# Kernel tuning notes

Measured on AMD Instinct MI355X. Metric: run time of the kernel, lower is better.

The kernel has to match this reference:

```python
import jax, jax.numpy as jnp
import numpy as np
import math

D_MODEL = 7168
NUM_HEADS = 128
Q_LORA = 1536
KV_LORA = 512
DN = 128   # qk_nope_head_dim
DR = 64    # qk_rope_head_dim
DV = 128   # v_head_dim
DQ = DN + DR  # q_head_dim = 192
ROPE_BASE = 10000.0


def _apply_rotary(t, cos, sin):
    """Faithful port of apply_rotary_pos_emb (interleaved even/odd split).
    t: [B,H,S,DR]; cos,sin: [S,DR]."""
    cos = cos[None, None]  # [1,1,S,DR]
    sin = sin[None, None]
    x1 = t[..., ::2]
    x2 = t[..., 1::2]
    c = cos[..., ::2]
    s = sin[..., ::2]
    rot = jnp.stack([x1 * c - x2 * s, x1 * s + x2 * c], axis=-1)
    return rot.reshape(t.shape)


def setup_inputs() -> dict:
    key = jax.random.key(0)
    ks = jax.random.split(key, 7)
    B, S = 1, 1024
    sc = 0.02  # small init to keep softmax well-conditioned
    hidden_states = jax.random.normal(ks[0], (B, S, D_MODEL), dtype=jnp.float32)
    Wqa = jax.random.normal(ks[1], (Q_LORA, D_MODEL), dtype=jnp.float32) * sc
    Wkva = jax.random.normal(ks[2], (KV_LORA, D_MODEL), dtype=jnp.float32) * sc
    Wqb = jax.random.normal(ks[3], (NUM_HEADS * DQ, Q_LORA), dtype=jnp.float32) * sc
    Wkb = jax.random.normal(ks[4], (NUM_HEADS * DQ, KV_LORA), dtype=jnp.float32) * sc
    Wvb = jax.random.normal(ks[5], (NUM_HEADS * DV, KV_LORA), dtype=jnp.float32) * sc
    Wo = jax.random.normal(ks[6], (D_MODEL, NUM_HEADS * DV), dtype=jnp.float32) * sc
    return {"hidden_states": hidden_states, "Wqa": Wqa, "Wkva": Wkva,
            "Wqb": Wqb, "Wkb": Wkb, "Wvb": Wvb, "Wo": Wo}


def reference(hidden_states, Wqa, Wkva, Wqb, Wkb, Wvb, Wo):
    B, S, _ = hidden_states.shape
    # low-rank latent projections
    q_lat = jnp.einsum('bsd,rd->bsr', hidden_states, Wqa)    # [B,S,Q_LORA]
    kv_lat = jnp.einsum('bsd,rd->bsr', hidden_states, Wkva)  # [B,S,KV_LORA]
    # per-head up-projections
    q = jnp.einsum('bsr,er->bse', q_lat, Wqb).reshape(B, S, NUM_HEADS, DQ).transpose(0, 2, 1, 3)
    k = jnp.einsum('bsr,er->bse', kv_lat, Wkb).reshape(B, S, NUM_HEADS, DQ).transpose(0, 2, 1, 3)
    v = jnp.einsum('bsr,er->bse', kv_lat, Wvb).reshape(B, S, NUM_HEADS, DV).transpose(0, 2, 1, 3)
    # RoPE tables (YaRoPE: emb = cat(freqs, freqs))
    pos = jnp.arange(S, dtype=jnp.float32)
    inv_freq = 1.0 / (ROPE_BASE ** (jnp.arange(0, DR, 2, dtype=jnp.float32) / DR))
    freqs = jnp.outer(pos, inv_freq)                  # [S, DR/2]
    emb = jnp.concatenate([freqs, freqs], axis=-1)    # [S, DR]
    cos, sin = jnp.cos(emb), jnp.sin(emb)
    # split nope / rope, rotate rope halves
    q_nope, q_rope = q[..., :DN], q[..., DN:]
    k_nope, k_rope = k[..., :DN], k[..., DN:]
    q_rope = _apply_rotary(q_rope, cos, sin)
    k_rope = _apply_rotary(k_rope, cos, sin)
    q = jnp.concatenate([q_nope, q_rope], axis=-1)
    k = jnp.concatenate([k_nope, k_rope], axis=-1)
    # attention (no mask: attention_mask=None path)
    scores = jnp.einsum('bhqd,bhkd->bhqk', q, k) / math.sqrt(DQ)
    attn = jax.nn.softmax(scores, axis=-1)
    out = jnp.einsum('bhqk,bhkd->bhqd', attn, v)      # [B,H,S,DV]
    out = out.transpose(0, 2, 1, 3).reshape(B, S, NUM_HEADS * DV)
    return jnp.einsum('bse,de->bsd', out, Wo)         # [B,S,D_MODEL]
```

## Files before the change

### kernel.cpp

```cpp
#include <hip/hip_runtime.h>

typedef short v8s __attribute__((ext_vector_type(8)));
typedef float v4f __attribute__((ext_vector_type(4)));

#define S_LEN 1024
#define NH    128
#define DM    7168
#define QL    1536
#define KVL   512
#define DQd   192
#define DVd   128
#define QDIM  (NH * DQd)
#define VDIM  (NH * DVd)

__device__ __forceinline__ float bf2f(unsigned short u) {
  union { unsigned int i; float f; } x; x.i = ((unsigned int)u) << 16; return x.f;
}
__device__ __forceinline__ unsigned short f2bf(float f) {
  union { float f; unsigned int i; } x; x.f = f;
  unsigned int r = x.i + 0x7fffu + ((x.i >> 16) & 1u);
  return (unsigned short)(r >> 16);
}
__device__ __forceinline__ v8s cvt8pair(v4f f0, v4f f1) {
  v8s r; unsigned short* u = (unsigned short*)&r;
#pragma unroll
  for (int i = 0; i < 4; i++) { u[i] = f2bf(f0[i]); u[4 + i] = f2bf(f1[i]); }
  return r;
}

__device__ __forceinline__ int swz_off(int row, int slot) {
  return row * 128 + ((slot ^ (row & 7)) << 4);
}

__global__ void cvt_bf16_kernel(const float* __restrict__ in,
                                unsigned short* __restrict__ out, int n8) {
  int i = blockIdx.x * blockDim.x + threadIdx.x;
  if (i >= n8) return;
  v4f f0 = *(const v4f*)(in + (size_t)i * 8);
  v4f f1 = *(const v4f*)(in + (size_t)i * 8 + 4);
  *(v8s*)(out + (size_t)i * 8) = cvt8pair(f0, f1);
}

template<bool CF32>
__global__ __launch_bounds__(256) void gemm_tile(
    const unsigned short* __restrict__ A, int lda,
    const float* __restrict__ W, int ldw,
    void* __restrict__ Cv, int ldc, int K)
{
  __shared__ __align__(16) unsigned short As[128 * 64];
  __shared__ __align__(16) unsigned short Bs[128 * 64];

  const int t    = threadIdx.x;
  const int lane = t & 63;
  const int wave = t >> 6;
  const int r15  = lane & 15;
  const int quad = lane >> 4;
  const int wm = wave >> 1, wn = wave & 1;
  const int mb = blockIdx.y * 128;
  const int nb = blockIdx.x * 128;

  const int srow  = t >> 3;
  const int sslot = t & 7;

  const unsigned short* aptr = A + (size_t)(mb + srow) * lda + sslot * 8;
  const float*          wptr = W + (size_t)(nb + srow) * ldw + sslot * 8;
  const size_t a32 = (size_t)32 * lda;
  const size_t w32 = (size_t)32 * ldw;

  v4f acc[4][4];
#pragma unroll
  for (int i = 0; i < 4; i++)
#pragma unroll
    for (int j = 0; j < 4; j++) acc[i][j] = (v4f){0.f, 0.f, 0.f, 0.f};

  v8s stA[4];
  v4f stB[8];
#pragma unroll
  for (int p = 0; p < 4; p++) stA[p] = *(const v8s*)(aptr + p * a32);
#pragma unroll
  for (int p = 0; p < 4; p++) {
    stB[2 * p]     = *(const v4f*)(wptr + p * w32);
    stB[2 * p + 1] = *(const v4f*)(wptr + p * w32 + 4);
  }

  for (int k0 = 0; k0 < K; k0 += 64) {
    __syncthreads();
#pragma unroll
    for (int p = 0; p < 4; p++)
      *(v8s*)((char*)As + swz_off(p * 32 + srow, sslot)) = stA[p];
#pragma unroll
    for (int p = 0; p < 4; p++)
      *(v8s*)((char*)Bs + swz_off(p * 32 + srow, sslot)) =
          cvt8pair(stB[2 * p], stB[2 * p + 1]);
    __syncthreads();

    if (k0 + 64 < K) {
#pragma unroll
      for (int p = 0; p < 4; p++)
        stA[p] = *(const v8s*)(aptr + p * a32 + k0 + 64);
#pragma unroll
      for (int p = 0; p < 4; p++) {
        stB[2 * p]     = *(const v4f*)(wptr + p * w32 + k0 + 64);
        stB[2 * p + 1] = *(const v4f*)(wptr + p * w32 + k0 + 64 + 4);
      }
    }

#pragma unroll
    for (int kk = 0; kk < 2; kk++) {
      const int cslot = kk * 4 + quad;
      v8s af[4], bf[4];
#pragma unroll
      for (int fm = 0; fm < 4; fm++)
        af[fm] = *(const v8s*)((char*)As + swz_off(wm * 64 + fm * 16 + r15, cslot));
#pragma unroll
      for (int fn = 0; fn < 4; fn++)
        bf[fn] = *(const v8s*)((char*)Bs + swz_off(wn * 64 + fn * 16 + r15, cslot));
#pragma unroll
      for (int fm = 0; fm < 4; fm++)
#pragma unroll
        for (int fn = 0; fn < 4; fn++)
          acc[fm][fn] = __builtin_amdgcn_mfma_f32_16x16x32_bf16(
              af[fm], bf[fn], acc[fm][fn], 0, 0, 0);
    }
  }

  const int mrow = mb + wm * 64 + quad * 4;
  const int ncol = nb + wn * 64 + r15;
#pragma unroll
  for (int fm = 0; fm < 4; fm++) {
#pragma unroll
    for (int r = 0; r < 4; r++) {
      const size_t crow = (size_t)(mrow + fm * 16 + r) * ldc + ncol;
      if constexpr (CF32) {
        float* C = (float*)Cv;
#pragma unroll
        for (int fn = 0; fn < 4; fn++) C[crow + fn * 16] = acc[fm][fn][r];
      } else {
        unsigned short* C = (unsigned short*)Cv;
#pragma unroll
        for (int fn = 0; fn < 4; fn++) C[crow + fn * 16] = f2bf(acc[fm][fn][r]);
      }
    }
  }
}

__global__ void rope_kernel(unsigned short* __restrict__ q,
                            unsigned short* __restrict__ k)
{
  int idx = blockIdx.x * blockDim.x + threadIdx.x;
  int i = idx & 31;
  int h = (idx >> 5) & (NH - 1);
  int s = idx >> 12;
  int j = (2 * i) & 31;
  float freq = powf(10000.0f, -(float)j / 32.0f);
  float ang = (float)s * freq;
  float c = cosf(ang), sn = sinf(ang);
  size_t base = (size_t)s * QDIM + h * DQd + 128 + 2 * i;

  float t0 = bf2f(q[base]), t1 = bf2f(q[base + 1]);
  q[base]     = f2bf(t0 * c - t1 * sn);
  q[base + 1] = f2bf(t0 * sn + t1 * c);

  t0 = bf2f(k[base]); t1 = bf2f(k[base + 1]);
  k[base]     = f2bf(t0 * c - t1 * sn);
  k[base + 1] = f2bf(t0 * sn + t1 * c);
}

__global__ __launch_bounds__(256) void attn_kernel(
    const unsigned short* __restrict__ qb,
    const unsigned short* __restrict__ kb,
    const unsigned short* __restrict__ vb,
    unsigned short* __restrict__ ao)
{
  __shared__ unsigned short p_lds[16][1048];
  __shared__ unsigned short v_lds[64][130];
  __shared__ float redbuf[4][16];
  __shared__ float rowmax[16];
  __shared__ float rowinv[16];

  const int h  = blockIdx.y;
  const int q0 = blockIdx.x * 16;
  const int t = threadIdx.x;
  const int lane = t & 63;
  const int wave = t >> 6;
  const int r15  = lane & 15;
  const int quad = lane >> 4;
  const float scale = 0.07216878364870323f;

  v8s afr[6];
  {
    const unsigned short* qrow = qb + (size_t)(q0 + r15) * QDIM + h * DQd + quad * 8;
#pragma unroll
    for (int kk = 0; kk < 6; kk++) afr[kk] = *(const v8s*)(qrow + kk * 32);
  }

  float vmax[4] = {-1e30f, -1e30f, -1e30f, -1e30f};
  for (int st = wave; st < 64; st += 4) {
    const int k0 = st * 16;
    const unsigned short* krow = kb + (size_t)(k0 + r15) * QDIM + h * DQd + quad * 8;
    v4f acc = {0.f, 0.f, 0.f, 0.f};
#pragma unroll
    for (int kk = 0; kk < 6; kk++) {
      v8s b = *(const v8s*)(krow + kk * 32);
      acc = __builtin_amdgcn_mfma_f32_16x16x32_bf16(afr[kk], b, acc, 0, 0, 0);
    }
#pragma unroll
    for (int r = 0; r < 4; r++) vmax[r] = fmaxf(vmax[r], acc[r]);
  }
#pragma unroll
  for (int mk = 1; mk < 16; mk <<= 1) {
#pragma unroll
    for (int r = 0; r < 4; r++) vmax[r] = fmaxf(vmax[r], __shfl_xor(vmax[r], mk));
  }
  if (r15 == 0) {
#pragma unroll
    for (int r = 0; r < 4; r++) redbuf[wave][quad * 4 + r] = vmax[r];
  }
  __syncthreads();
  if (t < 16) {
    float m = fmaxf(fmaxf(redbuf[0][t], redbuf[1][t]),
                    fmaxf(redbuf[2][t], redbuf[3][t]));
    rowmax[t] = m * scale;
  }
  __syncthreads();

  float mrow[4];
#pragma unroll
  for (int r = 0; r < 4; r++) mrow[r] = rowmax[quad * 4 + r];
  float vsum[4] = {0.f, 0.f, 0.f, 0.f};
  for (int st = wave; st < 64; st += 4) {
    const int k0 = st * 16;
    const unsigned short* krow = kb + (size_t)(k0 + r15) * QDIM + h * DQd + quad * 8;
    v4f acc = {0.f, 0.f, 0.f, 0.f};
#pragma unroll
    for (int kk = 0; kk < 6; kk++) {
      v8s b = *(const v8s*)(krow + kk * 32);
      acc = __builtin_amdgcn_mfma_f32_16x16x32_bf16(afr[kk], b, acc, 0, 0, 0);
    }
#pragma unroll
    for (int r = 0; r < 4; r++) {
      float p = __expf(acc[r] * scale - mrow[r]);
      unsigned short pb = f2bf(p);
      p_lds[quad * 4 + r][k0 + r15] = pb;
      vsum[r] += bf2f(pb);
    }
  }
#pragma unroll
  for (int mk = 1; mk < 16; mk <<= 1) {
#pragma unroll
    for (int r = 0; r < 4; r++) vsum[r] += __shfl_xor(vsum[r], mk);
  }
  if (r15 == 0) {
#pragma unroll
    for (int r = 0; r < 4; r++) redbuf[wave][quad * 4 + r] = vsum[r];
  }
  __syncthreads();
  if (t < 16) {
    rowinv[t] = 1.0f / (redbuf[0][t] + redbuf[1][t] + redbuf[2][t] + redbuf[3][t]);
  }

  v4f oacc0 = {0.f, 0.f, 0.f, 0.f};
  v4f oacc1 = {0.f, 0.f, 0.f, 0.f};
  for (int c = 0; c < 16; c++) {
    __syncthreads();
    for (int e = t; e < 64 * 64; e += 256) {
      int kk = e >> 6;
      int d2 = (e & 63) * 2;
      *(unsigned int*)(&v_lds[kk][d2]) =
          *(const unsigned int*)(vb + (size_t)(c * 64 + kk) * VDIM + h * DVd + d2);
    }
    __syncthreads();
#pragma unroll
    for (int ks = 0; ks < 2; ks++) {
      const int kb2 = c * 64 + ks * 32 + quad * 8;
      v8s af = *(const v8s*)(&p_lds[r15][kb2]);
      const int kl = ks * 32 + quad * 8;
#pragma unroll
      for (int ds = 0; ds < 2; ds++) {
        const int d0 = (wave * 2 + ds) * 16;
        v8s bfr;
        unsigned short* bp = (unsigned short*)&bfr;
#pragma unroll
        for (int j = 0; j < 8; j++) bp[j] = v_lds[kl + j][d0 + r15];
        if (ds == 0) oacc0 = __builtin_amdgcn_mfma_f32_16x16x32_bf16(af, bfr, oacc0, 0, 0, 0);
        else         oacc1 = __builtin_amdgcn_mfma_f32_16x16x32_bf16(af, bfr, oacc1, 0, 0, 0);
      }
    }
  }

#pragma unroll
  for (int ds = 0; ds < 2; ds++) {
    const int d0 = (wave * 2 + ds) * 16;
#pragma unroll
    for (int r = 0; r < 4; r++) {
      const int qi = quad * 4 + r;
      float v = (ds == 0 ? oacc0[r] : oacc1[r]) * rowinv[qi];
      ao[(size_t)(q0 + qi) * VDIM + h * DVd + d0 + r15] = f2bf(v);
    }
  }
}

extern "C" void kernel_launch(void* const* d_in, const int* in_sizes, int n_in,
                              void* d_out, int out_size, void* d_ws, size_t ws_size,
                              hipStream_t stream) {
  const float* hidden = (const float*)d_in[0];
  const float* Wqa  = (const float*)d_in[1];
  const float* Wkva = (const float*)d_in[2];
  const float* Wqb  = (const float*)d_in[3];
  const float* Wkb  = (const float*)d_in[4];
  const float* Wvb  = (const float*)d_in[5];
  const float* Wo   = (const float*)d_in[6];
  float* out = (float*)d_out;

  unsigned short* ws  = (unsigned short*)d_ws;
  unsigned short* lat = ws;
  unsigned short* qb  = lat + (size_t)S_LEN * 2048;
  unsigned short* kb  = qb  + (size_t)S_LEN * QDIM;
  unsigned short* vb  = kb  + (size_t)S_LEN * QDIM;
  unsigned short* ao  = vb  + (size_t)S_LEN * VDIM;
  unsigned short* hb  = ao  + (size_t)S_LEN * VDIM;

  dim3 blk(256);

  cvt_bf16_kernel<<<(S_LEN * DM / 8) / 256, blk, 0, stream>>>(hidden, hb, S_LEN * DM / 8);

  gemm_tile<false><<<dim3(QL / 128, S_LEN / 128), blk, 0, stream>>>(
      hb, DM, Wqa, DM, lat, 2048, DM);
  gemm_tile<false><<<dim3(KVL / 128, S_LEN / 128), blk, 0, stream>>>(
      hb, DM, Wkva, DM, lat + QL, 2048, DM);

  gemm_tile<false><<<dim3(QDIM / 128, S_LEN / 128), blk, 0, stream>>>(
      lat, 2048, Wqb, QL, qb, QDIM, QL);
  gemm_tile<false><<<dim3(QDIM / 128, S_LEN / 128), blk, 0, stream>>>(
      lat + QL, 2048, Wkb, KVL, kb, QDIM, KVL);
  gemm_tile<false><<<dim3(VDIM / 128, S_LEN / 128), blk, 0, stream>>>(
      lat + QL, 2048, Wvb, KVL, vb, VDIM, KVL);

  rope_kernel<<<(S_LEN * NH * 32) / 256, blk, 0, stream>>>(qb, kb);

  attn_kernel<<<dim3(S_LEN / 16, NH), blk, 0, stream>>>(qb, kb, vb, ao);

  gemm_tile<true><<<dim3(DM / 128, S_LEN / 128), blk, 0, stream>>>(
      ao, VDIM, Wo, VDIM, out, DM, VDIM);
}
```

Baseline: 2.348 ms.

## Transpose V and keep QK scores in registers to avoid recomputation

Adds a transpose kernel that writes V as [head, dim, seq], so the PV MFMA loop can load B fragments directly from global memory with vector loads. This removes the per-chunk LDS staging of V, its scalar strided LDS reads, and the barriers around them. The QK^T scores are now kept in 16 register tiles across the max pass and reused in the exp pass, so the second QK^T matmul is no longer recomputed. It also adds s_setprio hints around the MFMA blocks. The costs are higher register pressure, an extra transpose launch, and extra workspace.

Result: faster. 2.123 ms (-9.6%).

```diff
diff --git a/kernel.cpp b/kernel.cpp
--- a/kernel.cpp
+++ b/kernel.cpp
@@ -41,6 +41,23 @@
   *(v8s*)(out + (size_t)i * 8) = cvt8pair(f0, f1);
 }
 
+__global__ __launch_bounds__(256) void transpose_kernel(
+    const unsigned short* __restrict__ in, unsigned short* __restrict__ out)
+{
+  const int lane = threadIdx.x & 63;
+  const int wave = threadIdx.x >> 6;
+  const int e  = blockIdx.x * 256 + wave * 64 + lane;
+  const int s0 = blockIdx.y * 32;
+  unsigned short tmp[32];
+#pragma unroll
+  for (int j = 0; j < 32; j++)
+    tmp[j] = in[(size_t)(s0 + j) * VDIM + e];
+  unsigned short* op = out + (size_t)e * S_LEN + s0;
+#pragma unroll
+  for (int j = 0; j < 4; j++)
+    *(v8s*)(op + j * 8) = *(v8s*)(tmp + j * 8);
+}
+
 template<bool CF32>
 __global__ __launch_bounds__(256) void gemm_tile(
     const unsigned short* __restrict__ A, int lda,
@@ -108,19 +125,19 @@
 #pragma unroll
     for (int kk = 0; kk < 2; kk++) {
       const int cslot = kk * 4 + quad;
-      v8s af[4], bf[4];
+      v8s af[4], bfv[4];
 #pragma unroll
       for (int fm = 0; fm < 4; fm++)
         af[fm] = *(const v8s*)((char*)As + swz_off(wm * 64 + fm * 16 + r15, cslot));
 #pragma unroll
       for (int fn = 0; fn < 4; fn++)
-        bf[fn] = *(const v8s*)((char*)Bs + swz_off(wn * 64 + fn * 16 + r15, cslot));
+        bfv[fn] = *(const v8s*)((char*)Bs + swz_off(wn * 64 + fn * 16 + r15, cslot));
 #pragma unroll
       for (int fm = 0; fm < 4; fm++)
 #pragma unroll
         for (int fn = 0; fn < 4; fn++)
           acc[fm][fn] = __builtin_amdgcn_mfma_f32_16x16x32_bf16(
-              af[fm], bf[fn], acc[fm][fn], 0, 0, 0);
+              af[fm], bfv[fn], acc[fm][fn], 0, 0, 0);
     }
   }
 
@@ -169,11 +186,10 @@
 __global__ __launch_bounds__(256) void attn_kernel(
     const unsigned short* __restrict__ qb,
     const unsigned short* __restrict__ kb,
-    const unsigned short* __restrict__ vb,
+    const unsigned short* __restrict__ vt,
     unsigned short* __restrict__ ao)
 {
-  __shared__ unsigned short p_lds[16][1048];
-  __shared__ unsigned short v_lds[64][130];
+  __shared__ __align__(16) unsigned short p_lds[16][1048];
   __shared__ float redbuf[4][16];
   __shared__ float rowmax[16];
   __shared__ float rowinv[16];
@@ -194,16 +210,21 @@
     for (int kk = 0; kk < 6; kk++) afr[kk] = *(const v8s*)(qrow + kk * 32);
   }
 
+  v4f sreg[16];
   float vmax[4] = {-1e30f, -1e30f, -1e30f, -1e30f};
-  for (int st = wave; st < 64; st += 4) {
-    const int k0 = st * 16;
+#pragma unroll
+  for (int i = 0; i < 16; i++) {
+    const int k0 = (wave + i * 4) * 16;
     const unsigned short* krow = kb + (size_t)(k0 + r15) * QDIM + h * DQd + quad * 8;
     v4f acc = {0.f, 0.f, 0.f, 0.f};
+    __builtin_amdgcn_s_setprio(1);
 #pragma unroll
     for (int kk = 0; kk < 6; kk++) {
       v8s b = *(const v8s*)(krow + kk * 32);
       acc = __builtin_amdgcn_mfma_f32_16x16x32_bf16(afr[kk], b, acc, 0, 0, 0);
     }
+    __builtin_amdgcn_s_setprio(0);
+    sreg[i] = acc;
 #pragma unroll
     for (int r = 0; r < 4; r++) vmax[r] = fmaxf(vmax[r], acc[r]);
   }
@@ -228,18 +249,12 @@
 #pragma unroll
   for (int r = 0; r < 4; r++) mrow[r] = rowmax[quad * 4 + r];
   float vsum[4] = {0.f, 0.f, 0.f, 0.f};
-  for (int st = wave; st < 64; st += 4) {
-    const int k0 = st * 16;
-    const unsigned short* krow = kb + (size_t)(k0 + r15) * QDIM + h * DQd + quad * 8;
-    v4f acc = {0.f, 0.f, 0.f, 0.f};
-#pragma unroll
-    for (int kk = 0; kk < 6; kk++) {
-      v8s b = *(const v8s*)(krow + kk * 32);
-      acc = __builtin_amdgcn_mfma_f32_16x16x32_bf16(afr[kk], b, acc, 0, 0, 0);
-    }
+#pragma unroll
+  for (int i = 0; i < 16; i++) {
+    const int k0 = (wave + i * 4) * 16;
 #pragma unroll
     for (int r = 0; r < 4; r++) {
-      float p = __expf(acc[r] * scale - mrow[r]);
+      float p = __expf(sreg[i][r] * scale - mrow[r]);
       unsigned short pb = f2bf(p);
       p_lds[quad * 4 + r][k0 + r15] = pb;
       vsum[r] += bf2f(pb);
@@ -258,34 +273,22 @@
   if (t < 16) {
     rowinv[t] = 1.0f / (redbuf[0][t] + redbuf[1][t] + redbuf[2][t] + redbuf[3][t]);
   }
+  __syncthreads();
 
   v4f oacc0 = {0.f, 0.f, 0.f, 0.f};
   v4f oacc1 = {0.f, 0.f, 0.f, 0.f};
-  for (int c = 0; c < 16; c++) {
-    __syncthreads();
-    for (int e = t; e < 64 * 64; e += 256) {
-      int kk = e >> 6;
-      int d2 = (e & 63) * 2;
-      *(unsigned int*)(&v_lds[kk][d2]) =
-          *(const unsigned int*)(vb + (size_t)(c * 64 + kk) * VDIM + h * DVd + d2);
-    }
-    __syncthreads();
-#pragma unroll
-    for (int ks = 0; ks < 2; ks++) {
-      const int kb2 = c * 64 + ks * 32 + quad * 8;
-      v8s af = *(const v8s*)(&p_lds[r15][kb2]);
-      const int kl = ks * 32 + quad * 8;
-#pragma unroll
-      for (int ds = 0; ds < 2; ds++) {
-        const int d0 = (wave * 2 + ds) * 16;
-        v8s bfr;
-        unsigned short* bp = (unsigned short*)&bfr;
-#pragma unroll
-        for (int j = 0; j < 8; j++) bp[j] = v_lds[kl + j][d0 + r15];
-        if (ds == 0) oacc0 = __builtin_amdgcn_mfma_f32_16x16x32_bf16(af, bfr, oacc0, 0, 0, 0);
-        else         oacc1 = __builtin_amdgcn_mfma_f32_16x16x32_bf16(af, bfr, oacc1, 0, 0, 0);
-      }
-    }
+  const unsigned short* vbase = vt + (size_t)h * DVd * S_LEN;
+  const int d0a = (wave * 2) * 16 + r15;
+  const int d0b = (wave * 2 + 1) * 16 + r15;
+  for (int kt = 0; kt < 32; kt++) {
+    const int kk = kt * 32 + quad * 8;
+    v8s af  = *(const v8s*)(&p_lds[r15][kk]);
+    v8s bf0 = *(const v8s*)(vbase + (size_t)d0a * S_LEN + kk);
+    v8s bf1 = *(const v8s*)(vbase + (size_t)d0b * S_LEN + kk);
+    __builtin_amdgcn_s_setprio(1);
+    oacc0 = __builtin_amdgcn_mfma_f32_16x16x32_bf16(af, bf0, oacc0, 0, 0, 0);
+    oacc1 = __builtin_amdgcn_mfma_f32_16x16x32_bf16(af, bf1, oacc1, 0, 0, 0);
+    __builtin_amdgcn_s_setprio(0);
   }
 
 #pragma unroll
@@ -319,6 +322,7 @@
   unsigned short* vb  = kb  + (size_t)S_LEN * QDIM;
   unsigned short* ao  = vb  + (size_t)S_LEN * VDIM;
   unsigned short* hb  = ao  + (size_t)S_LEN * VDIM;
+  unsigned short* vt  = hb  + (size_t)S_LEN * DM;
 
   dim3 blk(256);
 
@@ -338,7 +342,9 @@
 
   rope_kernel<<<(S_LEN * NH * 32) / 256, blk, 0, stream>>>(qb, kb);
 
-  attn_kernel<<<dim3(S_LEN / 16, NH), blk, 0, stream>>>(qb, kb, vb, ao);
+  transpose_kernel<<<dim3(VDIM / 256, S_LEN / 32), blk, 0, stream>>>(vb, vt);
+
+  attn_kernel<<<dim3(S_LEN / 16, NH), blk, 0, stream>>>(qb, kb, vt, ao);
 
   gemm_tile<true><<<dim3(DM / 128, S_LEN / 128), blk, 0, stream>>>(
       ao, VDIM, Wo, VDIM, out, DM, VDIM);
```
